# Kernel tuning notes

Measured on AMD Instinct MI355X. Metric: run time of the kernel, lower is better.

## Reference

```python
import jax, jax.numpy as jnp
import numpy as np

D_MODEL = 1024
NUM_HEADS = 16
HEAD_DIM = D_MODEL // NUM_HEADS


def setup_inputs() -> dict:
    key = jax.random.key(0)
    ks = jax.random.split(key, 10)
    B, S, D = 2, 2048, D_MODEL
    s = 1.0 / np.sqrt(D)
    return {
        "x": jax.random.normal(ks[0], (B, S, D), dtype=jnp.float32),
        "q_w": jax.random.normal(ks[1], (D, D), dtype=jnp.float32) * s,
        "q_b": jnp.zeros((D,), dtype=jnp.float32),
        "k_w": jax.random.normal(ks[2], (D, D), dtype=jnp.float32) * s,
        "k_b": jnp.zeros((D,), dtype=jnp.float32),
        "v_w": jax.random.normal(ks[3], (D, D), dtype=jnp.float32) * s,
        "v_b": jnp.zeros((D,), dtype=jnp.float32),
        "out_w": jax.random.normal(ks[4], (D, D), dtype=jnp.float32) * s,
        "out_b": jnp.zeros((D,), dtype=jnp.float32),
        "evidence_scale": jnp.ones((1,), dtype=jnp.float32),
        "evidence_bias": jnp.zeros((1,), dtype=jnp.float32),
    }


def reference(x, q_w, q_b, k_w, k_b, v_w, v_b, out_w, out_b, evidence_scale, evidence_bias):
    B, S, D = x.shape
    H, Hd = NUM_HEADS, HEAD_DIM

    def proj(w, b):  # torch Linear: x @ w.T + b, then split heads -> [B,H,S,Hd]
        y = jnp.einsum('bsd,ed->bse', x, w) + b
        return y.reshape(B, S, H, Hd).transpose(0, 2, 1, 3)

    Q = proj(q_w, q_b)
    K = proj(k_w, k_b)
    V = proj(v_w, v_b)

    scores = jnp.einsum('bhqd,bhkd->bhqk', Q, K) / np.sqrt(Hd)  # [B,H,S,S]
    evidence = jnp.exp(scores) * evidence_scale + 1.0 + evidence_bias
    denom = evidence.sum(axis=-1, keepdims=True)                # [B,H,S,1]
    uncertainty = S / denom                                     # [B,H,S,1]
    probs = evidence / denom

    attn = jnp.einsum('bhqk,bhkd->bhqd', probs, V)              # [B,H,S,Hd]
    attn = attn.transpose(0, 2, 1, 3).reshape(B, S, D)
    output = jnp.einsum('bsd,ed->bse', attn, out_w) + out_b
    return output, jnp.squeeze(uncertainty, -1)
```

## Files before the change

### kernel.cpp

```cpp
#include <hip/hip_runtime.h>

typedef __attribute__((ext_vector_type(8))) short bf16x8;
typedef __attribute__((ext_vector_type(4))) float f32x4;
typedef __attribute__((ext_vector_type(4))) unsigned int u32x4;
typedef unsigned short ushort_t;

constexpr int Dm  = 1024;
constexpr int NH  = 16;
constexpr int HD  = 64;
constexpr int SQ  = 2048;
constexpr int BB  = 2;
constexpr int MM  = BB * SQ;

__device__ __forceinline__ ushort_t f2bf(float f) {
    unsigned int u = __float_as_uint(f);
    u += 0x7FFFu + ((u >> 16) & 1u);
    return (ushort_t)(u >> 16);
}

__device__ __forceinline__ void gld16(const void* g, void* l) {
    __builtin_amdgcn_global_load_lds(
        (const __attribute__((address_space(1))) void*)g,
        (__attribute__((address_space(3))) void*)l, 16, 0, 0);
}

__global__ void cast_all(const float4* __restrict__ x,  const float4* __restrict__ qw,
                         const float4* __restrict__ kw, const float4* __restrict__ vw,
                         const float4* __restrict__ ow,
                         uint2* __restrict__ xb,  uint2* __restrict__ qwb,
                         uint2* __restrict__ kwb, uint2* __restrict__ vwb,
                         uint2* __restrict__ owb)
{
    int i = blockIdx.x * 256 + threadIdx.x;
    const float4* src; uint2* dst; int off;
    if      (i < 1048576) { src = x;  dst = xb;  off = i; }
    else if (i < 1310720) { src = qw; dst = qwb; off = i - 1048576; }
    else if (i < 1572864) { src = kw; dst = kwb; off = i - 1310720; }
    else if (i < 1835008) { src = vw; dst = vwb; off = i - 1572864; }
    else                  { src = ow; dst = owb; off = i - 1835008; }
    float4 v = src[off];
    uint2 o;
    o.x = (unsigned)f2bf(v.x) | ((unsigned)f2bf(v.y) << 16);
    o.y = (unsigned)f2bf(v.z) | ((unsigned)f2bf(v.w) << 16);
    dst[off] = o;
}

template<int TM, typename EPI>
__device__ __forceinline__ void gemm_core(const ushort_t* __restrict__ A,
                                          const ushort_t* __restrict__ W,
                                          const float* __restrict__ bias,
                                          int n0, int m0, EPI epi)
{
    constexpr int AF = TM / 32;
    __shared__ ushort_t As[2][TM * 32];
    __shared__ ushort_t Ws[2][128 * 32];
    const int t    = threadIdx.x;
    const int lane = t & 63, w = t >> 6;
    const int lm   = lane & 15, quad = lane >> 4;
    const int wm   = w & 1, wn = w >> 1;

    const f32x4 fz = {0.f, 0.f, 0.f, 0.f};
    f32x4 acc[AF][4];
#pragma unroll
    for (int mi = 0; mi < AF; ++mi)
#pragma unroll
        for (int ni = 0; ni < 4; ++ni) acc[mi][ni] = fz;

    float bsv[4];
#pragma unroll
    for (int ni = 0; ni < 4; ++ni) bsv[ni] = bias[n0 + wn * 64 + ni * 16 + lm];

    auto stage = [&](int k0, int b) {
#pragma unroll
        for (int j = 0; j < TM / 64; ++j) {
            int s = t + 256 * j;
            gld16(A + (size_t)(m0 + (s >> 2)) * 1024 + k0 + (s & 3) * 8, &As[b][s * 8]);
        }
#pragma unroll
        for (int j = 0; j < 2; ++j) {
            int s = t + 256 * j;
            gld16(W + (size_t)(n0 + (s >> 2)) * 1024 + k0 + (s & 3) * 8, &Ws[b][s * 8]);
        }
    };

    stage(0, 0);
    int cur = 0;
    for (int k0 = 0; k0 < 1024; k0 += 32) {
        __syncthreads();
        if (k0 + 32 < 1024) stage(k0 + 32, cur ^ 1);

        bf16x8 af[AF], bfr[4];
#pragma unroll
        for (int mi = 0; mi < AF; ++mi)
            af[mi] = *(const bf16x8*)&As[cur][(wm * (TM / 2) + mi * 16 + lm) * 32 + quad * 8];
#pragma unroll
        for (int ni = 0; ni < 4; ++ni)
            bfr[ni] = *(const bf16x8*)&Ws[cur][(wn * 64 + ni * 16 + lm) * 32 + quad * 8];
#pragma unroll
        for (int mi = 0; mi < AF; ++mi)
#pragma unroll
            for (int ni = 0; ni < 4; ++ni)
                acc[mi][ni] = __builtin_amdgcn_mfma_f32_16x16x32_bf16(
                                  af[mi], bfr[ni], acc[mi][ni], 0, 0, 0);
        cur ^= 1;
    }

#pragma unroll
    for (int mi = 0; mi < AF; ++mi)
#pragma unroll
        for (int ni = 0; ni < 4; ++ni)
#pragma unroll
            for (int r = 0; r < 4; ++r) {
                const int m = m0 + wm * (TM / 2) + mi * 16 + quad * 4 + r;
                const int n = n0 + wn * 64 + ni * 16 + lm;
                epi(m, n, acc[mi][ni][r] + bsv[ni]);
            }
}

__global__ __launch_bounds__(256) void gemm_qkv(
    const ushort_t* __restrict__ xb,
    const ushort_t* __restrict__ qwb, const float* __restrict__ qb,
    const ushort_t* __restrict__ kwb, const float* __restrict__ kb,
    const ushort_t* __restrict__ vwb, const float* __restrict__ vb,
    ushort_t* __restrict__ Qb, ushort_t* __restrict__ Kb, ushort_t* __restrict__ Vb)
{
    const int z = blockIdx.z;
    const ushort_t* W   = (z == 0) ? qwb : (z == 1) ? kwb : vwb;
    const float*    bias = (z == 0) ? qb  : (z == 1) ? kb  : vb;
    ushort_t*       dst  = (z == 0) ? Qb  : (z == 1) ? Kb  : Vb;
    const int n0 = blockIdx.x * 128, m0 = blockIdx.y * 128;
    const bool vt = (z == 2);
    const float qs = (z == 0) ? 0.125f : 1.0f;

    gemm_core<128>(xb, W, bias, n0, m0, [&](int m, int n, float v) {
        v *= qs;
        const int b = m >> 11, s = m & 2047, h = n >> 6, hd = n & 63;
        const size_t idx = vt ? ((size_t)((b * NH + h) * 64 + hd) * SQ + s)
                              : ((size_t)((b * NH + h) * SQ + s) * 64 + hd);
        dst[idx] = f2bf(v);
    });
}

__global__ __launch_bounds__(256) void gemm_out(
    const ushort_t* __restrict__ Ab, const ushort_t* __restrict__ owb,
    const float* __restrict__ ob, float* __restrict__ out)
{
    const int n0 = blockIdx.x * 128, m0 = blockIdx.y * 64;
    gemm_core<64>(Ab, owb, ob, n0, m0, [&](int m, int n, float v) {
        out[(size_t)m * 1024 + n] = v;
    });
}

__global__ __launch_bounds__(256) void attn_mfma(const ushort_t* __restrict__ Qg,
                                                 const ushort_t* __restrict__ Kg,
                                                 const ushort_t* __restrict__ Vtg,
                                                 const float* __restrict__ esc,
                                                 const float* __restrict__ ebi,
                                                 ushort_t* __restrict__ Ab,
                                                 float* __restrict__ unc)
{
    __shared__ __align__(16) ushort_t Kbuf[2][4096];
    __shared__ __align__(16) ushort_t Vbuf[2][4096];

    const int t    = threadIdx.x;
    const int lane = t & 63, w = t >> 6;
    const int lm   = lane & 15, quad = lane >> 4;
    const int qt   = blockIdx.x & 31;
    const int bh   = blockIdx.x >> 5;
    const int q0   = qt * 64;

    const float scale = esc[0];
    const float bias1 = 1.0f + ebi[0];

    bf16x8 qa[2];
#pragma unroll
    for (int kc = 0; kc < 2; ++kc)
        qa[kc] = *(const bf16x8*)(Qg + (size_t)(bh * SQ + q0 + w * 16 + lm) * 64
                                  + kc * 32 + quad * 8);

    bf16x8 onesA;
#pragma unroll
    for (int j = 0; j < 8; ++j) onesA[j] = (short)0x3F80;

    const f32x4 fz = {0.f, 0.f, 0.f, 0.f};
    f32x4 acc[4];
#pragma unroll
    for (int nd = 0; nd < 4; ++nd) acc[nd] = fz;
    f32x4 acc1 = fz;

    const int vq = ((quad & 1) << 4) + ((quad >> 1) << 3);

    auto stage = [&](int kt, int b) {
        const ushort_t* kg = Kg + (size_t)(bh * SQ + kt * 64 + w * 16 + lm) * 64 + quad * 8;
        gld16(kg,      &Kbuf[b][(w * 2 + 0) * 512]);
        gld16(kg + 32, &Kbuf[b][(w * 2 + 1) * 512]);
        const ushort_t* vg = Vtg + (size_t)bh * 64 * SQ + (size_t)(w * 16 + lm) * SQ
                           + kt * 64 + vq;
        gld16(vg,      &Vbuf[b][(w * 2 + 0) * 512]);
        gld16(vg + 32, &Vbuf[b][(w * 2 + 1) * 512]);
    };

    stage(0, 0);
    int cur = 0;
    const bool odd = (quad & 1) != 0;
    for (int kt = 0; kt < 32; ++kt) {
        __syncthreads();
        if (kt + 1 < 32) stage(kt + 1, cur ^ 1);
        const ushort_t* Kc = Kbuf[cur];
        const ushort_t* Vc = Vbuf[cur];

#pragma unroll
        for (int hc = 0; hc < 2; ++hc) {
            f32x4 st0 = fz, st1 = fz;
#pragma unroll
            for (int kc = 0; kc < 2; ++kc) {
                bf16x8 kb0 = *(const bf16x8*)&Kc[((hc * 2 + 0) * 2 + kc) * 512 + lane * 8];
                bf16x8 kb1 = *(const bf16x8*)&Kc[((hc * 2 + 1) * 2 + kc) * 512 + lane * 8];
                st0 = __builtin_amdgcn_mfma_f32_16x16x32_bf16(kb0, qa[kc], st0, 0, 0, 0);
                st1 = __builtin_amdgcn_mfma_f32_16x16x32_bf16(kb1, qa[kc], st1, 0, 0, 0);
            }
            unsigned pk0[2], pk1[2];
#pragma unroll
            for (int p = 0; p < 2; ++p) {
                float a0 = fmaf(__expf(st0[2 * p]),     scale, bias1);
                float a1 = fmaf(__expf(st0[2 * p + 1]), scale, bias1);
                float b0 = fmaf(__expf(st1[2 * p]),     scale, bias1);
                float b1 = fmaf(__expf(st1[2 * p + 1]), scale, bias1);
                asm("v_cvt_pk_bf16_f32 %0, %1, %2" : "=v"(pk0[p]) : "v"(a0), "v"(a1));
                asm("v_cvt_pk_bf16_f32 %0, %1, %2" : "=v"(pk1[p]) : "v"(b0), "v"(b1));
            }
            unsigned keep0 = odd ? pk1[0] : pk0[0];
            unsigned keep1 = odd ? pk1[1] : pk0[1];
            unsigned send0 = odd ? pk0[0] : pk1[0];
            unsigned send1 = odd ? pk0[1] : pk1[1];
            unsigned recv0 = (unsigned)__builtin_amdgcn_ds_swizzle((int)send0, 0x401F);
            unsigned recv1 = (unsigned)__builtin_amdgcn_ds_swizzle((int)send1, 0x401F);
            u32x4 fv;
            fv[0] = odd ? recv0 : keep0;
            fv[1] = odd ? recv1 : keep1;
            fv[2] = odd ? keep0 : recv0;
            fv[3] = odd ? keep1 : recv1;
            bf16x8 eb = __builtin_bit_cast(bf16x8, fv);
#pragma unroll
            for (int nd = 0; nd < 4; ++nd) {
                bf16x8 va = *(const bf16x8*)&Vc[(nd * 2 + hc) * 512 + lane * 8];
                acc[nd] = __builtin_amdgcn_mfma_f32_16x16x32_bf16(va, eb, acc[nd], 0, 0, 0);
            }
            acc1 = __builtin_amdgcn_mfma_f32_16x16x32_bf16(onesA, eb, acc1, 0, 0, 0);
        }
        cur ^= 1;
    }

    const float di = 1.0f / acc1[0];
    if (quad == 0)
        unc[(size_t)bh * SQ + q0 + w * 16 + lm] = (float)SQ * di;

    const int b = bh >> 4, h = bh & 15;
    const size_t arow = (size_t)(b * SQ + q0 + w * 16 + lm) * Dm + h * 64;
#pragma unroll
    for (int nd = 0; nd < 4; ++nd) {
        float o0 = acc[nd][0] * di, o1 = acc[nd][1] * di;
        float o2 = acc[nd][2] * di, o3 = acc[nd][3] * di;
        unsigned lo, hi;
        asm("v_cvt_pk_bf16_f32 %0, %1, %2" : "=v"(lo) : "v"(o0), "v"(o1));
        asm("v_cvt_pk_bf16_f32 %0, %1, %2" : "=v"(hi) : "v"(o2), "v"(o3));
        uint2 ov; ov.x = lo; ov.y = hi;
        *(uint2*)&Ab[arow + nd * 16 + quad * 4] = ov;
    }
}

extern "C" void kernel_launch(void* const* d_in, const int* in_sizes, int n_in,
                              void* d_out, int out_size, void* d_ws, size_t ws_size,
                              hipStream_t stream)
{
    const float* x   = (const float*)d_in[0];
    const float* qw  = (const float*)d_in[1];
    const float* qb  = (const float*)d_in[2];
    const float* kw  = (const float*)d_in[3];
    const float* kb  = (const float*)d_in[4];
    const float* vw  = (const float*)d_in[5];
    const float* vb  = (const float*)d_in[6];
    const float* ow  = (const float*)d_in[7];
    const float* ob  = (const float*)d_in[8];
    const float* esc = (const float*)d_in[9];
    const float* ebi = (const float*)d_in[10];

    float* out = (float*)d_out;
    float* unc = out + (size_t)MM * Dm;

    ushort_t* xb  = (ushort_t*)d_ws;
    ushort_t* qwb = (ushort_t*)((char*)d_ws + (8u  << 20));
    ushort_t* kwb = (ushort_t*)((char*)d_ws + (10u << 20));
    ushort_t* vwb = (ushort_t*)((char*)d_ws + (12u << 20));
    ushort_t* owb = (ushort_t*)((char*)d_ws + (14u << 20));
    ushort_t* Vb  = (ushort_t*)((char*)d_ws + (16u << 20));
    ushort_t* Ab  = xb;

    ushort_t* Qb = (ushort_t*)d_out;
    ushort_t* Kb = Qb + (size_t)MM * Dm;

    cast_all<<<dim3(2097152 / 256), dim3(256), 0, stream>>>(
        (const float4*)x, (const float4*)qw, (const float4*)kw,
        (const float4*)vw, (const float4*)ow,
        (uint2*)xb, (uint2*)qwb, (uint2*)kwb, (uint2*)vwb, (uint2*)owb);

    gemm_qkv<<<dim3(Dm / 128, MM / 128, 3), dim3(256), 0, stream>>>(
        xb, qwb, qb, kwb, kb, vwb, vb, Qb, Kb, Vb);

    attn_mfma<<<dim3(BB * NH * (SQ / 64)), dim3(256), 0, stream>>>(
        Qb, Kb, Vb, esc, ebi, Ab, unc);

    gemm_out<<<dim3(Dm / 128, MM / 64), dim3(256), 0, stream>>>(Ab, owb, ob, out);
}
```

Before: 220.5 us.

## Process two query groups per wave in attention, halving block size

After: 240.2 us. +8.9%, slower.

```diff
diff --git a/kernel.cpp b/kernel.cpp
--- a/kernel.cpp
+++ b/kernel.cpp
@@ -151,7 +151,7 @@
     });
 }
 
-__global__ __launch_bounds__(256) void attn_mfma(const ushort_t* __restrict__ Qg,
+__global__ __launch_bounds__(128) void attn_mfma(const ushort_t* __restrict__ Qg,
                                                  const ushort_t* __restrict__ Kg,
                                                  const ushort_t* __restrict__ Vtg,
                                                  const float* __restrict__ esc,
@@ -172,32 +172,40 @@
     const float scale = esc[0];
     const float bias1 = 1.0f + ebi[0];
 
-    bf16x8 qa[2];
-#pragma unroll
-    for (int kc = 0; kc < 2; ++kc)
-        qa[kc] = *(const bf16x8*)(Qg + (size_t)(bh * SQ + q0 + w * 16 + lm) * 64
-                                  + kc * 32 + quad * 8);
+    bf16x8 qa[2][2];
+#pragma unroll
+    for (int qg = 0; qg < 2; ++qg)
+#pragma unroll
+        for (int kc = 0; kc < 2; ++kc)
+            qa[qg][kc] = *(const bf16x8*)(Qg + (size_t)(bh * SQ + q0 + w * 32 + qg * 16 + lm) * 64
+                                          + kc * 32 + quad * 8);
 
     bf16x8 onesA;
 #pragma unroll
     for (int j = 0; j < 8; ++j) onesA[j] = (short)0x3F80;
 
     const f32x4 fz = {0.f, 0.f, 0.f, 0.f};
-    f32x4 acc[4];
-#pragma unroll
-    for (int nd = 0; nd < 4; ++nd) acc[nd] = fz;
-    f32x4 acc1 = fz;
-
-    const int vq = ((quad & 1) << 4) + ((quad >> 1) << 3);
+    f32x4 acc[2][4];
+#pragma unroll
+    for (int qg = 0; qg < 2; ++qg)
+#pragma unroll
+        for (int nd = 0; nd < 4; ++nd) acc[qg][nd] = fz;
+    f32x4 acc1[2] = {fz, fz};
 
     auto stage = [&](int kt, int b) {
-        const ushort_t* kg = Kg + (size_t)(bh * SQ + kt * 64 + w * 16 + lm) * 64 + quad * 8;
-        gld16(kg,      &Kbuf[b][(w * 2 + 0) * 512]);
-        gld16(kg + 32, &Kbuf[b][(w * 2 + 1) * 512]);
-        const ushort_t* vg = Vtg + (size_t)bh * 64 * SQ + (size_t)(w * 16 + lm) * SQ
-                           + kt * 64 + vq;
-        gld16(vg,      &Vbuf[b][(w * 2 + 0) * 512]);
-        gld16(vg + 32, &Vbuf[b][(w * 2 + 1) * 512]);
+#pragma unroll
+        for (int j = 0; j < 4; ++j) {
+            const int s    = t + 128 * j;
+            const int bs   = s >> 6;
+            const int slm  = s & 15, squad = (s >> 4) & 3;
+            const int g    = bs >> 1, kc = bs & 1;
+            gld16(Kg + (size_t)(bh * SQ + kt * 64 + g * 16 + slm) * 64 + kc * 32 + squad * 8,
+                  &Kbuf[b][s * 8]);
+            const int svq  = ((squad & 1) << 4) + ((squad >> 1) << 3);
+            gld16(Vtg + (size_t)bh * 64 * SQ + (size_t)(g * 16 + slm) * SQ
+                      + kt * 64 + kc * 32 + svq,
+                  &Vbuf[b][s * 8]);
+        }
     };
 
     stage(0, 0);
@@ -211,61 +219,73 @@
 
 #pragma unroll
         for (int hc = 0; hc < 2; ++hc) {
-            f32x4 st0 = fz, st1 = fz;
+            f32x4 st[2][2];
+#pragma unroll
+            for (int qg = 0; qg < 2; ++qg) { st[qg][0] = fz; st[qg][1] = fz; }
 #pragma unroll
             for (int kc = 0; kc < 2; ++kc) {
                 bf16x8 kb0 = *(const bf16x8*)&Kc[((hc * 2 + 0) * 2 + kc) * 512 + lane * 8];
                 bf16x8 kb1 = *(const bf16x8*)&Kc[((hc * 2 + 1) * 2 + kc) * 512 + lane * 8];
-                st0 = __builtin_amdgcn_mfma_f32_16x16x32_bf16(kb0, qa[kc], st0, 0, 0, 0);
-                st1 = __builtin_amdgcn_mfma_f32_16x16x32_bf16(kb1, qa[kc], st1, 0, 0, 0);
+#pragma unroll
+                for (int qg = 0; qg < 2; ++qg) {
+                    st[qg][0] = __builtin_amdgcn_mfma_f32_16x16x32_bf16(kb0, qa[qg][kc], st[qg][0], 0, 0, 0);
+                    st[qg][1] = __builtin_amdgcn_mfma_f32_16x16x32_bf16(kb1, qa[qg][kc], st[qg][1], 0, 0, 0);
+                }
             }
-            unsigned pk0[2], pk1[2];
-#pragma unroll
-            for (int p = 0; p < 2; ++p) {
-                float a0 = fmaf(__expf(st0[2 * p]),     scale, bias1);
-                float a1 = fmaf(__expf(st0[2 * p + 1]), scale, bias1);
-                float b0 = fmaf(__expf(st1[2 * p]),     scale, bias1);
-                float b1 = fmaf(__expf(st1[2 * p + 1]), scale, bias1);
-                asm("v_cvt_pk_bf16_f32 %0, %1, %2" : "=v"(pk0[p]) : "v"(a0), "v"(a1));
-                asm("v_cvt_pk_bf16_f32 %0, %1, %2" : "=v"(pk1[p]) : "v"(b0), "v"(b1));
+            bf16x8 eb[2];
+#pragma unroll
+            for (int qg = 0; qg < 2; ++qg) {
+                unsigned pk0[2], pk1[2];
+#pragma unroll
+                for (int p = 0; p < 2; ++p) {
+                    float a0 = fmaf(__expf(st[qg][0][2 * p]),     scale, bias1);
+                    float a1 = fmaf(__expf(st[qg][0][2 * p + 1]), scale, bias1);
+                    float b0 = fmaf(__expf(st[qg][1][2 * p]),     scale, bias1);
+                    float b1 = fmaf(__expf(st[qg][1][2 * p + 1]), scale, bias1);
+                    asm("v_cvt_pk_bf16_f32 %0, %1, %2" : "=v"(pk0[p]) : "v"(a0), "v"(a1));
+                    asm("v_cvt_pk_bf16_f32 %0, %1, %2" : "=v"(pk1[p]) : "v"(b0), "v"(b1));
+                }
+                unsigned send0 = odd ? pk0[0] : pk1[0];
+                unsigned send1 = odd ? pk0[1] : pk1[1];
+                unsigned recv0 = (unsigned)__builtin_amdgcn_ds_swizzle((int)send0, 0x401F);
+                unsigned recv1 = (unsigned)__builtin_amdgcn_ds_swizzle((int)send1, 0x401F);
+                u32x4 fv;
+                fv[0] = odd ? recv0 : pk0[0];
+                fv[1] = odd ? recv1 : pk0[1];
+                fv[2] = odd ? pk1[0] : recv0;
+                fv[3] = odd ? pk1[1] : recv1;
+                eb[qg] = __builtin_bit_cast(bf16x8, fv);
             }
-            unsigned keep0 = odd ? pk1[0] : pk0[0];
-            unsigned keep1 = odd ? pk1[1] : pk0[1];
-            unsigned send0 = odd ? pk0[0] : pk1[0];
-            unsigned send1 = odd ? pk0[1] : pk1[1];
-            unsigned recv0 = (unsigned)__builtin_amdgcn_ds_swizzle((int)send0, 0x401F);
-            unsigned recv1 = (unsigned)__builtin_amdgcn_ds_swizzle((int)send1, 0x401F);
-            u32x4 fv;
-            fv[0] = odd ? recv0 : keep0;
-            fv[1] = odd ? recv1 : keep1;
-            fv[2] = odd ? keep0 : recv0;
-            fv[3] = odd ? keep1 : recv1;
-            bf16x8 eb = __builtin_bit_cast(bf16x8, fv);
 #pragma unroll
             for (int nd = 0; nd < 4; ++nd) {
                 bf16x8 va = *(const bf16x8*)&Vc[(nd * 2 + hc) * 512 + lane * 8];
-                acc[nd] = __builtin_amdgcn_mfma_f32_16x16x32_bf16(va, eb, acc[nd], 0, 0, 0);
+                acc[0][nd] = __builtin_amdgcn_mfma_f32_16x16x32_bf16(va, eb[0], acc[0][nd], 0, 0, 0);
+                acc[1][nd] = __builtin_amdgcn_mfma_f32_16x16x32_bf16(va, eb[1], acc[1][nd], 0, 0, 0);
             }
-            acc1 = __builtin_amdgcn_mfma_f32_16x16x32_bf16(onesA, eb, acc1, 0, 0, 0);
+            acc1[0] = __builtin_amdgcn_mfma_f32_16x16x32_bf16(onesA, eb[0], acc1[0], 0, 0, 0);
+            acc1[1] = __builtin_amdgcn_mfma_f32_16x16x32_bf16(onesA, eb[1], acc1[1], 0, 0, 0);
         }
         cur ^= 1;
     }
 
-    const float di = 1.0f / acc1[0];
-    if (quad == 0)
-        unc[(size_t)bh * SQ + q0 + w * 16 + lm] = (float)SQ * di;
-
     const int b = bh >> 4, h = bh & 15;
-    const size_t arow = (size_t)(b * SQ + q0 + w * 16 + lm) * Dm + h * 64;
-#pragma unroll
-    for (int nd = 0; nd < 4; ++nd) {
-        float o0 = acc[nd][0] * di, o1 = acc[nd][1] * di;
-        float o2 = acc[nd][2] * di, o3 = acc[nd][3] * di;
-        unsigned lo, hi;
-        asm("v_cvt_pk_bf16_f32 %0, %1, %2" : "=v"(lo) : "v"(o0), "v"(o1));
-        asm("v_cvt_pk_bf16_f32 %0, %1, %2" : "=v"(hi) : "v"(o2), "v"(o3));
-        uint2 ov; ov.x = lo; ov.y = hi;
-        *(uint2*)&Ab[arow + nd * 16 + quad * 4] = ov;
+#pragma unroll
+    for (int qg = 0; qg < 2; ++qg) {
+        const float di = 1.0f / acc1[qg][0];
+        if (quad == 0)
+            unc[(size_t)bh * SQ + q0 + w * 32 + qg * 16 + lm] = (float)SQ * di;
+
+        const size_t arow = (size_t)(b * SQ + q0 + w * 32 + qg * 16 + lm) * Dm + h * 64;
+#pragma unroll
+        for (int nd = 0; nd < 4; ++nd) {
+            float o0 = acc[qg][nd][0] * di, o1 = acc[qg][nd][1] * di;
+            float o2 = acc[qg][nd][2] * di, o3 = acc[qg][nd][3] * di;
+            unsigned lo, hi;
+            asm("v_cvt_pk_bf16_f32 %0, %1, %2" : "=v"(lo) : "v"(o0), "v"(o1));
+            asm("v_cvt_pk_bf16_f32 %0, %1, %2" : "=v"(hi) : "v"(o2), "v"(o3));
+            uint2 ov; ov.x = lo; ov.y = hi;
+            *(uint2*)&Ab[arow + nd * 16 + quad * 4] = ov;
+        }
     }
 }
 
@@ -307,7 +327,7 @@
     gemm_qkv<<<dim3(Dm / 128, MM / 128, 3), dim3(256), 0, stream>>>(
         xb, qwb, qb, kwb, kb, vwb, vb, Qb, Kb, Vb);
 
-    attn_mfma<<<dim3(BB * NH * (SQ / 64)), dim3(256), 0, stream>>>(
+    attn_mfma<<<dim3(BB * NH * (SQ / 64)), dim3(128), 0, stream>>>(
         Qb, Kb, Vb, esc, ebi, Ab, unc);
 
     gemm_out<<<dim3(Dm / 128, MM / 64), dim3(256), 0, stream>>>(Ab, owb, ob, out);
```
